# Kernel optimization log

Measured on AMD Instinct MI355X. Metric: run time of the kernel, lower is better.

The kernel has to match this reference:

```python
import jax, jax.numpy as jnp
import numpy as np

N_NODES = 50000
N_EDGES = 800000
D = 64


def setup_inputs() -> dict:
    key = jax.random.key(0)
    ks = jax.random.split(key, 8)
    x = jax.random.normal(ks[0], (N_NODES, D), dtype=jnp.float32)
    src = jax.random.randint(ks[1], (N_EDGES,), 0, N_NODES, dtype=jnp.int32)
    dst = jax.random.randint(ks[2], (N_EDGES,), 0, N_NODES, dtype=jnp.int32)
    s = 1.0 / np.sqrt(D)
    w1_0 = jax.random.uniform(ks[3], (D, D), jnp.float32, -s, s)
    w2_0 = jax.random.uniform(ks[4], (D, D), jnp.float32, -s, s)
    w1_1 = jax.random.uniform(ks[5], (D, D), jnp.float32, -s, s)
    w2_1 = jax.random.uniform(ks[6], (D, D), jnp.float32, -s, s)
    b = jnp.zeros((D,), jnp.float32)
    return {"x": x, "src": src, "dst": dst,
            "w1_0": w1_0, "b1_0": b, "w2_0": w2_0, "b2_0": b,
            "w1_1": w1_1, "b1_1": b, "w2_1": w2_1, "b2_1": b}


def _gin_layer(x, src, dst, w1, b1, w2, b2):
    # sum aggregation over edges: agg[i] = sum_{(j->i) in E} x[j]
    agg = jax.ops.segment_sum(x[src], dst, num_segments=N_NODES)
    h = x + agg  # (1 + eps) * x + agg, eps = 0 (DGL GINConv default)
    h = jnp.tanh(h @ w1 + b1)
    return h @ w2 + b2


def reference(x, src, dst, w1_0, b1_0, w2_0, b2_0, w1_1, b1_1, w2_1, b2_1):
    x = _gin_layer(x, src, dst, w1_0, b1_0, w2_0, b2_0)
    x = _gin_layer(x, src, dst, w1_1, b1_1, w2_1, b2_1)
    return x
```

## Files before the change

### kernel.cpp

```cpp
#include <hip/hip_runtime.h>

#define D 64
#define CAP 56
#define ACH 6250
#define LSLOT 3584

typedef __attribute__((ext_vector_type(8))) short short8;
typedef __attribute__((ext_vector_type(4))) float f32x4;

__device__ __forceinline__ unsigned short f2bf(float f) {
    unsigned u = __float_as_uint(f);
    u = (u + 0x7fff + ((u >> 16) & 1)) >> 16;
    return (unsigned short)u;
}
__device__ __forceinline__ float bf_lo(unsigned u) { return __uint_as_float(u << 16); }
__device__ __forceinline__ float bf_hi(unsigned u) { return __uint_as_float(u & 0xffff0000u); }

__global__ __launch_bounds__(256) void prep_scatter_kernel(
    const int* __restrict__ src, const int* __restrict__ dst,
    unsigned* __restrict__ gcur, unsigned* __restrict__ elog,
    int n_edges, int S, int nsb,
    const float* __restrict__ x, unsigned short* __restrict__ xb, int n4, int ncb,
    const float* __restrict__ w1_0, const float* __restrict__ w2_0,
    const float* __restrict__ w1_1, const float* __restrict__ w2_1,
    unsigned short* __restrict__ wt)
{
    __shared__ int cnt[784], start[784], cur[784], gb[784];
    __shared__ int wsum[4];
    __shared__ unsigned reorder[6272];

    const int b   = blockIdx.x;
    const int tid = threadIdx.x;

    if (b < nsb) {
        const int e0 = b * ACH;
        const int nE = (n_edges - e0 < ACH) ? (n_edges - e0) : ACH;

        for (int j = tid; j < 784; j += 256) cnt[j] = 0;
        __syncthreads();

        for (int i = tid; i < nE; i += 256)
            atomicAdd(&cnt[dst[e0 + i] >> 6], 1);
        __syncthreads();

        {
            int t4 = tid * 4;
            int c0 = 0, c1 = 0, c2 = 0, c3 = 0;
            if (t4 < 784) { c0 = cnt[t4]; c1 = cnt[t4+1]; c2 = cnt[t4+2]; c3 = cnt[t4+3]; }
            int lsum = c0 + c1 + c2 + c3;
            int lane = tid & 63, wv = tid >> 6;
            int xs = lsum;
            #pragma unroll
            for (int o = 1; o < 64; o <<= 1) {
                int y = __shfl_up(xs, o, 64);
                if (lane >= o) xs += y;
            }
            if (lane == 63) wsum[wv] = xs;
            __syncthreads();
            int wo = 0;
            for (int w = 0; w < wv; ++w) wo += wsum[w];
            int excl = wo + xs - lsum;
            if (t4 < 784) {
                start[t4]   = excl;              cur[t4]   = excl;
                start[t4+1] = excl + c0;         cur[t4+1] = excl + c0;
                start[t4+2] = excl + c0 + c1;    cur[t4+2] = excl + c0 + c1;
                start[t4+3] = excl + c0 + c1 + c2; cur[t4+3] = excl + c0 + c1 + c2;
            }
        }
        __syncthreads();

        for (int j = tid; j < S; j += 256) {
            int c = cnt[j];
            gb[j] = c ? (int)atomicAdd(&gcur[j], (unsigned)c) : 0;
        }

        for (int i = tid; i < nE; i += 256) {
            int d = dst[e0 + i];
            int s = src[e0 + i];
            int r = atomicAdd(&cur[d >> 6], 1);
            reorder[r] = ((unsigned)d << 16) | (unsigned)s;
        }
        __syncthreads();

        for (int i = tid; i < nE; i += 256) {
            unsigned v = reorder[i];
            int sl  = v >> 22;
            int idx = gb[sl] + (i - start[sl]);
            if (idx < LSLOT) elog[(size_t)sl * LSLOT + idx] = v;
        }
    } else if (b < nsb + ncb) {
        int i = (b - nsb) * 256 + tid;
        if (i < n4) {
            f32x4 v = __builtin_nontemporal_load((const f32x4*)(x + (size_t)i * 4));
            ushort4 o;
            o.x = f2bf(v.x); o.y = f2bf(v.y); o.z = f2bf(v.z); o.w = f2bf(v.w);
            *(ushort4*)(xb + (size_t)i * 4) = o;
        }
    } else {
        int i = (b - nsb - ncb) * 256 + tid;
        int m = i >> 12, r = i & 4095;
        int n = r >> 6, k = r & 63;
        const float* w = (m == 0) ? w1_0 : (m == 1) ? w2_0 : (m == 2) ? w1_1 : w2_1;
        wt[i] = f2bf(w[k * 64 + n]);
    }
}

__global__ __launch_bounds__(256) void bucketize_kernel(
    const unsigned* __restrict__ gcur, const unsigned* __restrict__ elog,
    int* __restrict__ deg, unsigned short* __restrict__ buf)
{
    __shared__ int sdeg[64];
    __shared__ unsigned short sbuf[64][CAP];

    const int g   = blockIdx.x;
    const int tid = threadIdx.x;

    unsigned* zb = (unsigned*)&sbuf[0][0];
    for (int i = tid; i < 64 * CAP / 2; i += 256) zb[i] = 0;
    if (tid < 64) sdeg[tid] = 0;
    int cnt = (int)gcur[g]; if (cnt > LSLOT) cnt = LSLOT;
    __syncthreads();

    for (int i = tid; i < cnt; i += 256) {
        unsigned v = elog[(size_t)g * LSLOT + i];
        int dl = (v >> 16) & 63;
        int p  = atomicAdd(&sdeg[dl], 1);
        if (p < CAP) sbuf[dl][p] = (unsigned short)(v & 0xffffu);
    }
    __syncthreads();

    const unsigned* sb = (const unsigned*)&sbuf[0][0];
    unsigned* gbuf = (unsigned*)(buf + (size_t)g * 64 * CAP);
    for (int i = tid; i < 64 * CAP / 2; i += 256) gbuf[i] = sb[i];
    if (tid < 64) deg[g * 64 + tid] = sdeg[tid];
}

__global__ __launch_bounds__(256) void gather_kernel(
    const unsigned short* __restrict__ xb, const int* __restrict__ deg,
    const unsigned short* __restrict__ buf, unsigned short* __restrict__ aggb)
{
    const int tid  = threadIdx.x;
    const int lane = tid & 63;
    const int wave = tid >> 6;
    const int n    = blockIdx.x * 4 + wave;

    const int slot = lane >> 3;
    const int fc   = (lane & 7) << 3;

    int my_idx = buf[(size_t)n * CAP + (lane < CAP ? lane : CAP - 1)];
    int dd = deg[n];
    dd = dd < CAP ? dd : CAP;

    uint4 u = make_uint4(0u, 0u, 0u, 0u);
    if (slot == 0) u = *(const uint4*)(xb + (size_t)n * D + fc);

    int s[7];
    #pragma unroll
    for (int g = 0; g < 7; ++g) s[g] = __shfl(my_idx, (g << 3) + slot);

    uint4 v0 = *(const uint4*)(xb + (size_t)s[0] * D + fc);
    uint4 v1 = *(const uint4*)(xb + (size_t)s[1] * D + fc);
    uint4 v2 = *(const uint4*)(xb + (size_t)s[2] * D + fc);

    float a[8] = {0.f, 0.f, 0.f, 0.f, 0.f, 0.f, 0.f, 0.f};

    if (dd > 24) {
        #pragma unroll
        for (int g = 3; g < 7; ++g) {
            uint4 v = *(const uint4*)(xb + (size_t)s[g] * D + fc);
            float m = ((g << 3) + slot) < dd ? 1.0f : 0.0f;
            a[0] += bf_lo(v.x) * m; a[1] += bf_hi(v.x) * m;
            a[2] += bf_lo(v.y) * m; a[3] += bf_hi(v.y) * m;
            a[4] += bf_lo(v.z) * m; a[5] += bf_hi(v.z) * m;
            a[6] += bf_lo(v.w) * m; a[7] += bf_hi(v.w) * m;
        }
    }

    {
        float m0 = (slot      < dd) ? 1.0f : 0.0f;
        float m1 = (slot +  8 < dd) ? 1.0f : 0.0f;
        float m2 = (slot + 16 < dd) ? 1.0f : 0.0f;
        a[0] += bf_lo(v0.x) * m0 + bf_lo(v1.x) * m1 + bf_lo(v2.x) * m2 + bf_lo(u.x);
        a[1] += bf_hi(v0.x) * m0 + bf_hi(v1.x) * m1 + bf_hi(v2.x) * m2 + bf_hi(u.x);
        a[2] += bf_lo(v0.y) * m0 + bf_lo(v1.y) * m1 + bf_lo(v2.y) * m2 + bf_lo(u.y);
        a[3] += bf_hi(v0.y) * m0 + bf_hi(v1.y) * m1 + bf_hi(v2.y) * m2 + bf_hi(u.y);
        a[4] += bf_lo(v0.z) * m0 + bf_lo(v1.z) * m1 + bf_lo(v2.z) * m2 + bf_lo(u.z);
        a[5] += bf_hi(v0.z) * m0 + bf_hi(v1.z) * m1 + bf_hi(v2.z) * m2 + bf_hi(u.z);
        a[6] += bf_lo(v0.w) * m0 + bf_lo(v1.w) * m1 + bf_lo(v2.w) * m2 + bf_lo(u.w);
        a[7] += bf_hi(v0.w) * m0 + bf_hi(v1.w) * m1 + bf_hi(v2.w) * m2 + bf_hi(u.w);
    }

    #pragma unroll
    for (int m = 8; m <= 32; m <<= 1) {
        #pragma unroll
        for (int q = 0; q < 8; ++q) a[q] += __shfl_xor(a[q], m);
    }
    if (slot == 0) {
        uint4 o;
        o.x = (unsigned)f2bf(a[0]) | ((unsigned)f2bf(a[1]) << 16);
        o.y = (unsigned)f2bf(a[2]) | ((unsigned)f2bf(a[3]) << 16);
        o.z = (unsigned)f2bf(a[4]) | ((unsigned)f2bf(a[5]) << 16);
        o.w = (unsigned)f2bf(a[6]) | ((unsigned)f2bf(a[7]) << 16);
        *(uint4*)(aggb + (size_t)n * D + fc) = o;
    }
}

template <bool WRITE_BF16>
__global__ __launch_bounds__(256) void gin_dense_mfma(
    const unsigned short* __restrict__ hb, int n_nodes,
    const unsigned short* __restrict__ w1t, const float* __restrict__ b1,
    const unsigned short* __restrict__ w2t, const float* __restrict__ b2,
    float* __restrict__ out_f, unsigned short* __restrict__ out_b)
{
    __shared__ unsigned short sh [64][72];
    __shared__ unsigned short st [64][72];
    __shared__ unsigned short sw1[64][72];
    __shared__ unsigned short sw2[64][72];

    const int t    = threadIdx.x;
    const int lane = t & 63;
    const int wave = t >> 6;
    const int quad = lane >> 4;
    const int col  = lane & 15;
    const int nb   = blockIdx.x * 64;

    for (int c = t; c < 512; c += 256) {
        int row = c >> 3, c8 = (c & 7) << 3;
        *(uint4*)&sh [row][c8] = *(const uint4*)(hb  + (size_t)(nb + row) * D + c8);
        *(uint4*)&sw1[row][c8] = *(const uint4*)(w1t + row * D + c8);
        *(uint4*)&sw2[row][c8] = *(const uint4*)(w2t + row * D + c8);
    }
    __syncthreads();

    const int arow = 16 * wave + col;
    const int koff = quad << 3;

    short8 a0 = *(const short8*)&sh[arow][koff];
    short8 a1 = *(const short8*)&sh[arow][32 + koff];

    #pragma unroll
    for (int nt = 0; nt < 4; ++nt) {
        int n = (nt << 4) + col;
        short8 bw0 = *(const short8*)&sw1[n][koff];
        short8 bw1 = *(const short8*)&sw1[n][32 + koff];
        float bv = b1[n];
        f32x4 c = {bv, bv, bv, bv};
        c = __builtin_amdgcn_mfma_f32_16x16x32_bf16(a0, bw0, c, 0, 0, 0);
        c = __builtin_amdgcn_mfma_f32_16x16x32_bf16(a1, bw1, c, 0, 0, 0);
        #pragma unroll
        for (int r = 0; r < 4; ++r)
            st[16 * wave + (quad << 2) + r][n] = f2bf(tanhf(c[r]));
    }

    short8 p0 = *(const short8*)&st[arow][koff];
    short8 p1 = *(const short8*)&st[arow][32 + koff];

    #pragma unroll
    for (int nt = 0; nt < 4; ++nt) {
        int n = (nt << 4) + col;
        short8 bw0 = *(const short8*)&sw2[n][koff];
        short8 bw1 = *(const short8*)&sw2[n][32 + koff];
        float bv = b2[n];
        f32x4 c = {bv, bv, bv, bv};
        c = __builtin_amdgcn_mfma_f32_16x16x32_bf16(p0, bw0, c, 0, 0, 0);
        c = __builtin_amdgcn_mfma_f32_16x16x32_bf16(p1, bw1, c, 0, 0, 0);
        #pragma unroll
        for (int r = 0; r < 4; ++r) {
            int row = nb + 16 * wave + (quad << 2) + r;
            if (WRITE_BF16) {
                out_b[(size_t)row * D + n] = f2bf(c[r]);
            } else if (row < n_nodes) {
                out_f[(size_t)row * D + n] = c[r];
            }
        }
    }
}

extern "C" void kernel_launch(void* const* d_in, const int* in_sizes, int n_in,
                              void* d_out, int out_size, void* d_ws, size_t ws_size,
                              hipStream_t stream)
{
    const float* x    = (const float*)d_in[0];
    const int*   src  = (const int*)  d_in[1];
    const int*   dst  = (const int*)  d_in[2];
    const float* w1_0 = (const float*)d_in[3];
    const float* b1_0 = (const float*)d_in[4];
    const float* w2_0 = (const float*)d_in[5];
    const float* b2_0 = (const float*)d_in[6];
    const float* w1_1 = (const float*)d_in[7];
    const float* b1_1 = (const float*)d_in[8];
    const float* w2_1 = (const float*)d_in[9];
    const float* b2_1 = (const float*)d_in[10];
    float* out = (float*)d_out;

    const int n_nodes = in_sizes[0] / D;
    const int n_edges = in_sizes[1];
    const int n_pad   = (n_nodes + 63) & ~63;
    const int S       = n_pad >> 6;

    unsigned*       gcur = (unsigned*)d_ws;
    unsigned*       elog = gcur + S;
    int*            deg  = (int*)(elog + (size_t)S * LSLOT);
    unsigned short* buf  = (unsigned short*)(deg + n_pad);
    unsigned short* aggb = buf  + (size_t)n_pad * CAP;
    unsigned short* xb   = aggb + (size_t)n_pad * D;
    unsigned short* x1b  = xb   + (size_t)n_pad * D;
    unsigned short* wt   = x1b  + (size_t)n_pad * D;

    const int n4  = n_nodes * D / 4;
    const int ncb = (n4 + 255) / 256;
    const int nsb = (n_edges + ACH - 1) / ACH;

    hipMemsetAsync(gcur, 0, (size_t)S * sizeof(unsigned), stream);
    prep_scatter_kernel<<<nsb + ncb + 64, 256, 0, stream>>>(
        src, dst, gcur, elog, n_edges, S, nsb,
        x, xb, n4, ncb,
        w1_0, w2_0, w1_1, w2_1, wt);
    bucketize_kernel<<<S, 256, 0, stream>>>(gcur, elog, deg, buf);

    const int gather_blocks = n_nodes / 4;
    const int dense_blocks  = n_pad / 64;

    gather_kernel<<<gather_blocks, 256, 0, stream>>>(xb, deg, buf, aggb);
    gin_dense_mfma<true><<<dense_blocks, 256, 0, stream>>>(
        aggb, n_nodes, wt, b1_0, wt + 4096, b2_0, nullptr, x1b);
    gather_kernel<<<gather_blocks, 256, 0, stream>>>(x1b, deg, buf, aggb);
    gin_dense_mfma<false><<<dense_blocks, 256, 0, stream>>>(
        aggb, n_nodes, wt + 8192, b1_1, wt + 12288, b2_1, out, nullptr);
}
```

Measured before the change: 170.1 us.

## Fuse neighbor gather with dense MLP into one per-64-node kernel

Merges the gather kernel and the MFMA dense kernel so each block aggregates 64 nodes into shared memory, then runs both matmuls on them directly. This drops the aggregated-feature round trip through global memory and two launches per forward pass. It also loads the third neighbor group only when degree exceeds 16, and zero-pads the bf16 input up to the padded node count so padded rows are valid. The cost is fewer blocks (782 versus 12500) with each wave serially processing 16 nodes, which may reduce latency hiding in the gather phase.

```diff
diff --git a/kernel.cpp b/kernel.cpp
--- a/kernel.cpp
+++ b/kernel.cpp
@@ -20,7 +20,8 @@
     const int* __restrict__ src, const int* __restrict__ dst,
     unsigned* __restrict__ gcur, unsigned* __restrict__ elog,
     int n_edges, int S, int nsb,
-    const float* __restrict__ x, unsigned short* __restrict__ xb, int n4, int ncb,
+    const float* __restrict__ x, unsigned short* __restrict__ xb,
+    int n4, int n4p, int ncb,
     const float* __restrict__ w1_0, const float* __restrict__ w2_0,
     const float* __restrict__ w1_1, const float* __restrict__ w2_1,
     unsigned short* __restrict__ wt)
@@ -61,9 +62,9 @@
             for (int w = 0; w < wv; ++w) wo += wsum[w];
             int excl = wo + xs - lsum;
             if (t4 < 784) {
-                start[t4]   = excl;              cur[t4]   = excl;
-                start[t4+1] = excl + c0;         cur[t4+1] = excl + c0;
-                start[t4+2] = excl + c0 + c1;    cur[t4+2] = excl + c0 + c1;
+                start[t4]   = excl;                cur[t4]   = excl;
+                start[t4+1] = excl + c0;           cur[t4+1] = excl + c0;
+                start[t4+2] = excl + c0 + c1;      cur[t4+2] = excl + c0 + c1;
                 start[t4+3] = excl + c0 + c1 + c2; cur[t4+3] = excl + c0 + c1 + c2;
             }
         }
@@ -95,6 +96,8 @@
             ushort4 o;
             o.x = f2bf(v.x); o.y = f2bf(v.y); o.z = f2bf(v.z); o.w = f2bf(v.w);
             *(ushort4*)(xb + (size_t)i * 4) = o;
+        } else if (i < n4p) {
+            *(ushort4*)(xb + (size_t)i * 4) = make_ushort4(0, 0, 0, 0);
         }
     } else {
         int i = (b - nsb - ncb) * 256 + tid;
@@ -135,108 +138,108 @@
     if (tid < 64) deg[g * 64 + tid] = sdeg[tid];
 }
 
-__global__ __launch_bounds__(256) void gather_kernel(
-    const unsigned short* __restrict__ xb, const int* __restrict__ deg,
-    const unsigned short* __restrict__ buf, unsigned short* __restrict__ aggb)
+template <bool WRITE_BF16>
+__global__ __launch_bounds__(256) void gin_fused(
+    const unsigned short* __restrict__ xin,
+    const int* __restrict__ deg, const unsigned short* __restrict__ buf,
+    const unsigned short* __restrict__ w1t, const float* __restrict__ b1,
+    const unsigned short* __restrict__ w2t, const float* __restrict__ b2,
+    float* __restrict__ out_f, unsigned short* __restrict__ out_b, int n_nodes)
 {
-    const int tid  = threadIdx.x;
-    const int lane = tid & 63;
-    const int wave = tid >> 6;
-    const int n    = blockIdx.x * 4 + wave;
-
+    __shared__ __align__(16) unsigned short accb[64][72];
+    __shared__ __align__(16) unsigned short st  [64][72];
+    __shared__ __align__(16) unsigned short sw1 [64][72];
+    __shared__ __align__(16) unsigned short sw2 [64][72];
+
+    const int g    = blockIdx.x;
+    const int t    = threadIdx.x;
+    const int lane = t & 63;
+    const int wv   = t >> 6;
     const int slot = lane >> 3;
     const int fc   = (lane & 7) << 3;
 
-    int my_idx = buf[(size_t)n * CAP + (lane < CAP ? lane : CAP - 1)];
-    int dd = deg[n];
-    dd = dd < CAP ? dd : CAP;
-
-    uint4 u = make_uint4(0u, 0u, 0u, 0u);
-    if (slot == 0) u = *(const uint4*)(xb + (size_t)n * D + fc);
-
-    int s[7];
-    #pragma unroll
-    for (int g = 0; g < 7; ++g) s[g] = __shfl(my_idx, (g << 3) + slot);
-
-    uint4 v0 = *(const uint4*)(xb + (size_t)s[0] * D + fc);
-    uint4 v1 = *(const uint4*)(xb + (size_t)s[1] * D + fc);
-    uint4 v2 = *(const uint4*)(xb + (size_t)s[2] * D + fc);
-
-    float a[8] = {0.f, 0.f, 0.f, 0.f, 0.f, 0.f, 0.f, 0.f};
-
-    if (dd > 24) {
+    for (int c = t; c < 512; c += 256) {
+        int row = c >> 3, c8 = (c & 7) << 3;
+        *(uint4*)&sw1[row][c8] = *(const uint4*)(w1t + row * D + c8);
+        *(uint4*)&sw2[row][c8] = *(const uint4*)(w2t + row * D + c8);
+    }
+
+    #pragma unroll 2
+    for (int j = 0; j < 16; ++j) {
+        const int nl = (wv << 4) + j;
+        const int n  = (g << 6) + nl;
+
+        int my_idx = buf[(size_t)n * CAP + (lane < CAP ? lane : CAP - 1)];
+        int dd = deg[n];
+        dd = dd < CAP ? dd : CAP;
+
+        uint4 u = make_uint4(0u, 0u, 0u, 0u);
+        if (slot == 0) u = *(const uint4*)(xin + (size_t)n * D + fc);
+
+        int s[7];
         #pragma unroll
-        for (int g = 3; g < 7; ++g) {
-            uint4 v = *(const uint4*)(xb + (size_t)s[g] * D + fc);
-            float m = ((g << 3) + slot) < dd ? 1.0f : 0.0f;
-            a[0] += bf_lo(v.x) * m; a[1] += bf_hi(v.x) * m;
-            a[2] += bf_lo(v.y) * m; a[3] += bf_hi(v.y) * m;
-            a[4] += bf_lo(v.z) * m; a[5] += bf_hi(v.z) * m;
-            a[6] += bf_lo(v.w) * m; a[7] += bf_hi(v.w) * m;
-        }
-    }
-
-    {
-        float m0 = (slot      < dd) ? 1.0f : 0.0f;
-        float m1 = (slot +  8 < dd) ? 1.0f : 0.0f;
-        float m2 = (slot + 16 < dd) ? 1.0f : 0.0f;
-        a[0] += bf_lo(v0.x) * m0 + bf_lo(v1.x) * m1 + bf_lo(v2.x) * m2 + bf_lo(u.x);
-        a[1] += bf_hi(v0.x) * m0 + bf_hi(v1.x) * m1 + bf_hi(v2.x) * m2 + bf_hi(u.x);
-        a[2] += bf_lo(v0.y) * m0 + bf_lo(v1.y) * m1 + bf_lo(v2.y) * m2 + bf_lo(u.y);
-        a[3] += bf_hi(v0.y) * m0 + bf_hi(v1.y) * m1 + bf_hi(v2.y) * m2 + bf_hi(u.y);
-        a[4] += bf_lo(v0.z) * m0 + bf_lo(v1.z) * m1 + bf_lo(v2.z) * m2 + bf_lo(u.z);
-        a[5] += bf_hi(v0.z) * m0 + bf_hi(v1.z) * m1 + bf_hi(v2.z) * m2 + bf_hi(u.z);
-        a[6] += bf_lo(v0.w) * m0 + bf_lo(v1.w) * m1 + bf_lo(v2.w) * m2 + bf_lo(u.w);
-        a[7] += bf_hi(v0.w) * m0 + bf_hi(v1.w) * m1 + bf_hi(v2.w) * m2 + bf_hi(u.w);
-    }
-
-    #pragma unroll
-    for (int m = 8; m <= 32; m <<= 1) {
+        for (int gg = 0; gg < 7; ++gg) s[gg] = __shfl(my_idx, (gg << 3) + slot);
+
+        uint4 v0 = *(const uint4*)(xin + (size_t)s[0] * D + fc);
+        uint4 v1 = *(const uint4*)(xin + (size_t)s[1] * D + fc);
+
+        float a[8] = {0.f, 0.f, 0.f, 0.f, 0.f, 0.f, 0.f, 0.f};
+
+        if (dd > 16) {
+            uint4 v2 = *(const uint4*)(xin + (size_t)s[2] * D + fc);
+            float m2 = (slot + 16 < dd) ? 1.0f : 0.0f;
+            a[0] += bf_lo(v2.x) * m2; a[1] += bf_hi(v2.x) * m2;
+            a[2] += bf_lo(v2.y) * m2; a[3] += bf_hi(v2.y) * m2;
+            a[4] += bf_lo(v2.z) * m2; a[5] += bf_hi(v2.z) * m2;
+            a[6] += bf_lo(v2.w) * m2; a[7] += bf_hi(v2.w) * m2;
+        }
+        if (dd > 24) {
+            #pragma unroll
+            for (int gg = 3; gg < 7; ++gg) {
+                uint4 v = *(const uint4*)(xin + (size_t)s[gg] * D + fc);
+                float m = ((gg << 3) + slot) < dd ? 1.0f : 0.0f;
+                a[0] += bf_lo(v.x) * m; a[1] += bf_hi(v.x) * m;
+                a[2] += bf_lo(v.y) * m; a[3] += bf_hi(v.y) * m;
+                a[4] += bf_lo(v.z) * m; a[5] += bf_hi(v.z) * m;
+                a[6] += bf_lo(v.w) * m; a[7] += bf_hi(v.w) * m;
+            }
+        }
+        {
+            float m0 = (slot     < dd) ? 1.0f : 0.0f;
+            float m1 = (slot + 8 < dd) ? 1.0f : 0.0f;
+            a[0] += bf_lo(v0.x) * m0 + bf_lo(v1.x) * m1 + bf_lo(u.x);
+            a[1] += bf_hi(v0.x) * m0 + bf_hi(v1.x) * m1 + bf_hi(u.x);
+            a[2] += bf_lo(v0.y) * m0 + bf_lo(v1.y) * m1 + bf_lo(u.y);
+            a[3] += bf_hi(v0.y) * m0 + bf_hi(v1.y) * m1 + bf_hi(u.y);
+            a[4] += bf_lo(v0.z) * m0 + bf_lo(v1.z) * m1 + bf_lo(u.z);
+            a[5] += bf_hi(v0.z) * m0 + bf_hi(v1.z) * m1 + bf_hi(u.z);
+            a[6] += bf_lo(v0.w) * m0 + bf_lo(v1.w) * m1 + bf_lo(u.w);
+            a[7] += bf_hi(v0.w) * m0 + bf_hi(v1.w) * m1 + bf_hi(u.w);
+        }
+
         #pragma unroll
-        for (int q = 0; q < 8; ++q) a[q] += __shfl_xor(a[q], m);
-    }
-    if (slot == 0) {
-        uint4 o;
-        o.x = (unsigned)f2bf(a[0]) | ((unsigned)f2bf(a[1]) << 16);
-        o.y = (unsigned)f2bf(a[2]) | ((unsigned)f2bf(a[3]) << 16);
-        o.z = (unsigned)f2bf(a[4]) | ((unsigned)f2bf(a[5]) << 16);
-        o.w = (unsigned)f2bf(a[6]) | ((unsigned)f2bf(a[7]) << 16);
-        *(uint4*)(aggb + (size_t)n * D + fc) = o;
-    }
-}
-
-template <bool WRITE_BF16>
-__global__ __launch_bounds__(256) void gin_dense_mfma(
-    const unsigned short* __restrict__ hb, int n_nodes,
-    const unsigned short* __restrict__ w1t, const float* __restrict__ b1,
-    const unsigned short* __restrict__ w2t, const float* __restrict__ b2,
-    float* __restrict__ out_f, unsigned short* __restrict__ out_b)
-{
-    __shared__ unsigned short sh [64][72];
-    __shared__ unsigned short st [64][72];
-    __shared__ unsigned short sw1[64][72];
-    __shared__ unsigned short sw2[64][72];
-
-    const int t    = threadIdx.x;
-    const int lane = t & 63;
-    const int wave = t >> 6;
+        for (int m = 8; m <= 32; m <<= 1) {
+            #pragma unroll
+            for (int q = 0; q < 8; ++q) a[q] += __shfl_xor(a[q], m);
+        }
+        if (slot == 0) {
+            uint4 o;
+            o.x = (unsigned)f2bf(a[0]) | ((unsigned)f2bf(a[1]) << 16);
+            o.y = (unsigned)f2bf(a[2]) | ((unsigned)f2bf(a[3]) << 16);
+            o.z = (unsigned)f2bf(a[4]) | ((unsigned)f2bf(a[5]) << 16);
+            o.w = (unsigned)f2bf(a[6]) | ((unsigned)f2bf(a[7]) << 16);
+            *(uint4*)&accb[nl][fc] = o;
+        }
+    }
+    __syncthreads();
+
     const int quad = lane >> 4;
     const int col  = lane & 15;
-    const int nb   = blockIdx.x * 64;
-
-    for (int c = t; c < 512; c += 256) {
-        int row = c >> 3, c8 = (c & 7) << 3;
-        *(uint4*)&sh [row][c8] = *(const uint4*)(hb  + (size_t)(nb + row) * D + c8);
-        *(uint4*)&sw1[row][c8] = *(const uint4*)(w1t + row * D + c8);
-        *(uint4*)&sw2[row][c8] = *(const uint4*)(w2t + row * D + c8);
-    }
-    __syncthreads();
-
-    const int arow = 16 * wave + col;
+    const int arow = (wv << 4) + col;
     const int koff = quad << 3;
 
-    short8 a0 = *(const short8*)&sh[arow][koff];
-    short8 a1 = *(const short8*)&sh[arow][32 + koff];
+    short8 a0 = *(const short8*)&accb[arow][koff];
+    short8 a1 = *(const short8*)&accb[arow][32 + koff];
 
     #pragma unroll
     for (int nt = 0; nt < 4; ++nt) {
@@ -249,7 +252,7 @@
         c = __builtin_amdgcn_mfma_f32_16x16x32_bf16(a1, bw1, c, 0, 0, 0);
         #pragma unroll
         for (int r = 0; r < 4; ++r)
-            st[16 * wave + (quad << 2) + r][n] = f2bf(tanhf(c[r]));
+            st[(wv << 4) + (quad << 2) + r][n] = f2bf(tanhf(c[r]));
     }
 
     short8 p0 = *(const short8*)&st[arow][koff];
@@ -266,7 +269,7 @@
         c = __builtin_amdgcn_mfma_f32_16x16x32_bf16(p1, bw1, c, 0, 0, 0);
         #pragma unroll
         for (int r = 0; r < 4; ++r) {
-            int row = nb + 16 * wave + (quad << 2) + r;
+            int row = (g << 6) + (wv << 4) + (quad << 2) + r;
             if (WRITE_BF16) {
                 out_b[(size_t)row * D + n] = f2bf(c[r]);
             } else if (row < n_nodes) {
@@ -302,29 +305,24 @@
     unsigned*       elog = gcur + S;
     int*            deg  = (int*)(elog + (size_t)S * LSLOT);
     unsigned short* buf  = (unsigned short*)(deg + n_pad);
-    unsigned short* aggb = buf  + (size_t)n_pad * CAP;
-    unsigned short* xb   = aggb + (size_t)n_pad * D;
-    unsigned short* x1b  = xb   + (size_t)n_pad * D;
-    unsigned short* wt   = x1b  + (size_t)n_pad * D;
+    unsigned short* xb   = buf + (size_t)n_pad * CAP;
+    unsigned short* x1b  = xb  + (size_t)n_pad * D;
+    unsigned short* wt   = x1b + (size_t)n_pad * D;
 
     const int n4  = n_nodes * D / 4;
-    const int ncb = (n4 + 255) / 256;
+    const int n4p = n_pad * D / 4;
+    const int ncb = (n4p + 255) / 256;
     const int nsb = (n_edges + ACH - 1) / ACH;
 
     hipMemsetAsync(gcur, 0, (size_t)S * sizeof(unsigned), stream);
     prep_scatter_kernel<<<nsb + ncb + 64, 256, 0, stream>>>(
         src, dst, gcur, elog, n_edges, S, nsb,
-        x, xb, n4, ncb,
+        x, xb, n4, n4p, ncb,
         w1_0, w2_0, w1_1, w2_1, wt);
     bucketize_kernel<<<S, 256, 0, stream>>>(gcur, elog, deg, buf);
 
-    const int gather_blocks = n_nodes / 4;
-    const int dense_blocks  = n_pad / 64;
-
-    gather_kernel<<<gather_blocks, 256, 0, stream>>>(xb, deg, buf, aggb);
-    gin_dense_mfma<true><<<dense_blocks, 256, 0, stream>>>(
-        aggb, n_nodes, wt, b1_0, wt + 4096, b2_0, nullptr, x1b);
-    gather_kernel<<<gather_blocks, 256, 0, stream>>>(x1b, deg, buf, aggb);
-    gin_dense_mfma<false><<<dense_blocks, 256, 0, stream>>>(
-        aggb, n_nodes, wt + 8192, b1_1, wt + 12288, b2_1, out, nullptr);
-}
+    gin_fused<true><<<S, 256, 0, stream>>>(
+        xb, deg, buf, wt, b1_0, wt + 4096, b2_0, nullptr, x1b, n_nodes);
+    gin_fused<false><<<S, 256, 0, stream>>>(
+        x1b, deg, buf, wt + 8192, b1_1, wt + 12288, b2_1, out, nullptr, n_nodes);
+}
```

Result: slower. 181.9 us (+6.9%).
